# Kernel tuning notes

Hardware: AMD Instinct MI355X
Metric: run time of the kernel (lower is better)

## Reference

```python
import jax, jax.numpy as jnp
import numpy as np

N_NODES = 50000
N_EDGES = 640000
D = 128


def setup_inputs() -> dict:
    key = jax.random.key(0)
    ks = jax.random.split(key, 8)
    nfeats = jax.random.normal(ks[0], (N_NODES, 1, D), dtype=jnp.float32)
    efeats = jax.random.normal(ks[1], (N_EDGES, 1, D), dtype=jnp.float32)
    # Linear params (PyTorch convention: weight [out, in])
    W_msg_w = jax.random.normal(ks[2], (D, 2 * D), dtype=jnp.float32) * 0.05
    W_msg_b = jax.random.normal(ks[3], (D,), dtype=jnp.float32) * 0.05
    W_apply_w = jax.random.normal(ks[4], (D, 2 * D), dtype=jnp.float32) * 0.05
    W_apply_b = jax.random.normal(ks[5], (D,), dtype=jnp.float32) * 0.05
    src = jax.random.randint(ks[6], (N_EDGES,), 0, N_NODES, dtype=jnp.int32)
    dst = jax.random.randint(ks[7], (N_EDGES,), 0, N_NODES, dtype=jnp.int32)
    return {
        "nfeats": nfeats, "efeats": efeats,
        "W_msg_w": W_msg_w, "W_msg_b": W_msg_b,
        "W_apply_w": W_apply_w, "W_apply_b": W_apply_b,
        "src": src, "dst": dst,
    }


def reference(nfeats, efeats, W_msg_w, W_msg_b, W_apply_w, W_apply_b, src, dst):
    n_nodes = nfeats.shape[0]
    # message: W_msg(cat[src_h, edge_h])  -> [E, 1, D_out]
    msg_in = jnp.concatenate([nfeats[src], efeats], axis=-1)  # [E,1,2D]
    m = jnp.einsum("eqi,oi->eqo", msg_in, W_msg_w) + W_msg_b
    # segment-mean over destination nodes (DGL fn.mean; zero for isolated nodes)
    sums = jax.ops.segment_sum(m, dst, num_segments=n_nodes)  # [N,1,D]
    counts = jax.ops.segment_sum(jnp.ones((m.shape[0],), m.dtype), dst,
                                 num_segments=n_nodes)  # [N]
    h_neigh = sums / jnp.maximum(counts, 1.0)[:, None, None]
    # apply: relu(W_apply(cat[h, h_neigh]))
    upd_in = jnp.concatenate([nfeats, h_neigh], axis=-1)  # [N,1,2D]
    out = jax.nn.relu(jnp.einsum("nqi,oi->nqo", upd_in, W_apply_w) + W_apply_b)
    return out
```

## Files before the change

kernel.cpp:

```cpp
#include <hip/hip_runtime.h>

#define D 128
#define TWO_D 256
#define LDSR 264

typedef __attribute__((ext_vector_type(4))) float f32x4;
typedef __attribute__((ext_vector_type(8))) short bf16x8;

static __device__ __forceinline__ unsigned short f2bf(float x) {
  union { float f; unsigned u; } v; v.f = x;
  unsigned r = (v.u + 0x7fffu + ((v.u >> 16) & 1u)) >> 16;
  return (unsigned short)r;
}

__global__ void prep_pack(const float* __restrict__ wmsg,
                          const float* __restrict__ wapp,
                          unsigned short* __restrict__ Wp,
                          int* __restrict__ counts, int n_nodes) {
  int p = blockIdx.x * blockDim.x + threadIdx.x;
  int j = p & 7;
  int lane = (p >> 3) & 63;
  int ot = (p >> 9) & 7;
  int k0i = (p >> 12) & 7;
  int g = p >> 15;
  int o = ot * 16 + (lane & 15);
  int k = k0i * 32 + (lane >> 4) * 8 + j;
  const float* W = g ? wapp : wmsg;
  Wp[p] = f2bf(W[o * 256 + k]);
  if (p < n_nodes) counts[p] = 0;
}

__global__ void hist_kernel(const int* __restrict__ dst, int* __restrict__ counts,
                            int n_edges) {
  int e = blockIdx.x * blockDim.x + threadIdx.x;
  if (e < n_edges) atomicAdd(&counts[dst[e]], 1);
}

__global__ void scan_kernel(const int* __restrict__ counts, int* __restrict__ offsets,
                            int* __restrict__ cursor, int n, int n_edges) {
  __shared__ int lds[1024];
  int t = threadIdx.x;
  int C = (n + 1023) / 1024;
  int beg = t * C;
  int end = beg + C; if (end > n) end = n;
  int s = 0;
  for (int i = beg; i < end; ++i) s += counts[i];
  lds[t] = s;
  __syncthreads();
  for (int off = 1; off < 1024; off <<= 1) {
    int v = (t >= off) ? lds[t - off] : 0;
    __syncthreads();
    lds[t] += v;
    __syncthreads();
  }
  int run = (t == 0) ? 0 : lds[t - 1];
  for (int i = beg; i < end; ++i) {
    offsets[i] = run;
    cursor[i] = run;
    run += counts[i];
  }
  if (t == 1023) offsets[n] = n_edges;
}

__global__ void scatter_kernel(const int* __restrict__ dst, int* __restrict__ cursor,
                               int* __restrict__ edge_list, int n_edges) {
  int e = blockIdx.x * blockDim.x + threadIdx.x;
  if (e < n_edges) {
    int p = atomicAdd(&cursor[dst[e]], 1);
    edge_list[p] = e;
  }
}

__global__ __launch_bounds__(256) void gather_kernel(
    const float* __restrict__ nfeats, const float* __restrict__ efeats,
    const int* __restrict__ src, const int* __restrict__ edge_list,
    const int* __restrict__ offsets, unsigned short* __restrict__ X1,
    int n_nodes) {
  int w = (blockIdx.x * 256 + threadIdx.x) >> 6;
  int lane = threadIdx.x & 63;
  if (w >= n_nodes) return;
  int beg = offsets[w], end = offsets[w + 1];
  int cnt = end - beg;
  const f32x4* nf4 = (const f32x4*)nfeats;
  const f32x4* ef4 = (const f32x4*)efeats;
  const int c32 = lane & 31;
  const int slot = lane >> 5;
  f32x4 accn = (f32x4){0.f, 0.f, 0.f, 0.f};
  f32x4 acce = (f32x4){0.f, 0.f, 0.f, 0.f};

  for (int j0 = beg; j0 < end; j0 += 64) {
    int nj = end - j0; if (nj > 64) nj = 64;
    int e = 0, s = 0;
    if (lane < nj) { e = edge_list[j0 + lane]; s = src[e]; }
    for (int p = 0; p < nj; p += 4) {
      int i0 = p + slot;
      int i1 = p + 2 + slot;
      int ee0 = __shfl(e, i0), ss0 = __shfl(s, i0);
      int ee1 = __shfl(e, i1), ss1 = __shfl(s, i1);
      bool v0 = i0 < nj, v1 = i1 < nj;
      f32x4 a0, b0, a1, b1;
      if (v0) {
        a0 = nf4[(size_t)ss0 * 32 + c32];
        b0 = __builtin_nontemporal_load(&ef4[(size_t)ee0 * 32 + c32]);
      }
      if (v1) {
        a1 = nf4[(size_t)ss1 * 32 + c32];
        b1 = __builtin_nontemporal_load(&ef4[(size_t)ee1 * 32 + c32]);
      }
      if (v0) { accn += a0; acce += b0; }
      if (v1) { accn += a1; acce += b1; }
    }
  }
  #pragma unroll
  for (int k = 0; k < 4; ++k) {
    accn[k] += __shfl_xor(accn[k], 32);
    acce[k] += __shfl_xor(acce[k], 32);
  }
  float inv = (cnt > 0) ? 1.0f / (float)cnt : 0.0f;
  f32x4 v = (lane < 32) ? accn : acce;
  ushort4 o;
  o.x = f2bf(v[0] * inv); o.y = f2bf(v[1] * inv);
  o.z = f2bf(v[2] * inv); o.w = f2bf(v[3] * inv);
  ((ushort4*)(X1 + (size_t)w * TWO_D))[lane] = o;
}

__global__ __launch_bounds__(256) void node_gemm(
    const unsigned short* __restrict__ X1,
    const unsigned short* __restrict__ Wp,
    const float* __restrict__ b1,
    const float* __restrict__ b2,
    const float* __restrict__ nfeats,
    const int* __restrict__ offsets,
    float* __restrict__ out,
    int n_nodes) {
  __shared__ unsigned short xt[64 * LDSR];
  __shared__ int cnts[64];
  const int tid = threadIdx.x;
  const int base = blockIdx.x * 64;

  if (tid < 64) {
    int g = base + tid;
    cnts[tid] = (g < n_nodes) ? (offsets[g + 1] - offsets[g]) : 0;
  }
  #pragma unroll
  for (int it = 0; it < 8; ++it) {
    int chunk = tid + it * 256;
    int r = chunk >> 5, c = chunk & 31;
    int g = base + r;
    uint4 v = make_uint4(0, 0, 0, 0);
    if (g < n_nodes) v = ((const uint4*)X1)[(size_t)g * 32 + c];
    *(uint4*)&xt[r * LDSR + c * 8] = v;
  }
  __syncthreads();

  const int lane = tid & 63;
  const int wid = tid >> 6;
  const int m16 = lane & 15;
  const int quad = lane >> 4;
  const int arow = wid * 16 + m16;
  const int lane8 = lane << 3;

  f32x4 acc[8];
  #pragma unroll
  for (int ot = 0; ot < 8; ++ot) acc[ot] = (f32x4){0.f, 0.f, 0.f, 0.f};

  #pragma unroll
  for (int k0i = 0; k0i < 8; ++k0i) {
    bf16x8 a = *(const bf16x8*)&xt[arow * LDSR + k0i * 32 + quad * 8];
    #pragma unroll
    for (int ot = 0; ot < 8; ++ot) {
      bf16x8 b = *(const bf16x8*)&Wp[((k0i * 8 + ot) << 9) + lane8];
      acc[ot] = __builtin_amdgcn_mfma_f32_16x16x32_bf16(a, b, acc[ot], 0, 0, 0);
    }
  }
  __syncthreads();

  #pragma unroll
  for (int ot = 0; ot < 8; ++ot) {
    int o = ot * 16 + m16;
    float bias = b1[o];
    #pragma unroll
    for (int r = 0; r < 4; ++r) {
      int m = wid * 16 + quad * 4 + r;
      float h = acc[ot][r] + (cnts[m] > 0 ? bias : 0.0f);
      xt[m * LDSR + 128 + o] = f2bf(h);
    }
  }
  #pragma unroll
  for (int it = 0; it < 8; ++it) {
    int chunk = tid + it * 256;
    int r = chunk >> 5, c = chunk & 31;
    int g = base + r;
    float4 v = make_float4(0.f, 0.f, 0.f, 0.f);
    if (g < n_nodes) v = ((const float4*)nfeats)[(size_t)g * 32 + c];
    ushort4 bv;
    bv.x = f2bf(v.x); bv.y = f2bf(v.y); bv.z = f2bf(v.z); bv.w = f2bf(v.w);
    *(ushort4*)&xt[r * LDSR + c * 4] = bv;
  }
  __syncthreads();

  #pragma unroll
  for (int ot = 0; ot < 8; ++ot) acc[ot] = (f32x4){0.f, 0.f, 0.f, 0.f};

  #pragma unroll
  for (int k0i = 0; k0i < 8; ++k0i) {
    bf16x8 a = *(const bf16x8*)&xt[arow * LDSR + k0i * 32 + quad * 8];
    #pragma unroll
    for (int ot = 0; ot < 8; ++ot) {
      bf16x8 b = *(const bf16x8*)&Wp[32768 + ((k0i * 8 + ot) << 9) + lane8];
      acc[ot] = __builtin_amdgcn_mfma_f32_16x16x32_bf16(a, b, acc[ot], 0, 0, 0);
    }
  }
  #pragma unroll
  for (int ot = 0; ot < 8; ++ot) {
    int o = ot * 16 + m16;
    float bias = b2[o];
    #pragma unroll
    for (int r = 0; r < 4; ++r) {
      int m = wid * 16 + quad * 4 + r;
      int g = base + m;
      if (g < n_nodes) {
        float v = acc[ot][r] + bias;
        out[(size_t)g * D + o] = v > 0.f ? v : 0.f;
      }
    }
  }
}

extern "C" void kernel_launch(void* const* d_in, const int* in_sizes, int n_in,
                              void* d_out, int out_size, void* d_ws, size_t ws_size,
                              hipStream_t stream) {
  const float* nfeats = (const float*)d_in[0];
  const float* efeats = (const float*)d_in[1];
  const float* Wmsg_f = (const float*)d_in[2];
  const float* b1     = (const float*)d_in[3];
  const float* Wapp_f = (const float*)d_in[4];
  const float* b2     = (const float*)d_in[5];
  const int*   src    = (const int*)d_in[6];
  const int*   dst    = (const int*)d_in[7];
  const int n_nodes = in_sizes[0] / D;
  const int n_edges = in_sizes[6];

  char* ws = (char*)d_ws;
  size_t off = 0;
  unsigned short* X1 = (unsigned short*)(ws + off); off += (size_t)n_nodes * TWO_D * 2;
  unsigned short* Wp = (unsigned short*)(ws + off); off += (size_t)2 * D * TWO_D * 2;
  int* counts    = (int*)(ws + off); off += (size_t)n_nodes * 4;
  int* offsets   = (int*)(ws + off); off += (size_t)(n_nodes + 1) * 4;
  int* cursor    = (int*)(ws + off); off += (size_t)n_nodes * 4;
  int* edge_list = (int*)(ws + off); off += (size_t)n_edges * 4;
  (void)ws_size; (void)n_in; (void)out_size;

  prep_pack<<<256, 256, 0, stream>>>(Wmsg_f, Wapp_f, Wp, counts, n_nodes);
  hist_kernel<<<(n_edges + 255) / 256, 256, 0, stream>>>(dst, counts, n_edges);
  scan_kernel<<<1, 1024, 0, stream>>>(counts, offsets, cursor, n_nodes, n_edges);
  scatter_kernel<<<(n_edges + 255) / 256, 256, 0, stream>>>(dst, cursor, edge_list, n_edges);
  gather_kernel<<<(n_nodes + 3) / 4, 256, 0, stream>>>(nfeats, efeats, src, edge_list, offsets, X1, n_nodes);
  node_gemm<<<(n_nodes + 63) / 64, 256, 0, stream>>>(X1, Wp, b1, b2, nfeats, offsets, (float*)d_out, n_nodes);
}
```

Baseline: 689.4 us.

## Fuse gather into node GEMM and reuse histogram atomics for CSR scatter

Merges the per-node gather/mean kernel into the node GEMM kernel, so the mean features are written straight to shared memory and the intermediate bf16 X1 buffer round trip through global memory goes away. The histogram pass now records each edge's atomic rank, so the scatter needs no second atomic pass and no cursor array. Edge ids are stored together with their src index as int2 pairs, which removes the dependent src lookup in the gather loop. The trade-off is lower parallelism in the gather phase: each wave now handles 16 nodes in sequence inside a block that also holds a large LDS tile, which may reduce latency hiding.

```diff
diff --git a/kernel.cpp b/kernel.cpp
--- a/kernel.cpp
+++ b/kernel.cpp
@@ -30,14 +30,14 @@
   if (p < n_nodes) counts[p] = 0;
 }
 
-__global__ void hist_kernel(const int* __restrict__ dst, int* __restrict__ counts,
-                            int n_edges) {
+__global__ void hist_rank_kernel(const int* __restrict__ dst, int* __restrict__ counts,
+                                 int* __restrict__ rank, int n_edges) {
   int e = blockIdx.x * blockDim.x + threadIdx.x;
-  if (e < n_edges) atomicAdd(&counts[dst[e]], 1);
+  if (e < n_edges) rank[e] = atomicAdd(&counts[dst[e]], 1);
 }
 
 __global__ void scan_kernel(const int* __restrict__ counts, int* __restrict__ offsets,
-                            int* __restrict__ cursor, int n, int n_edges) {
+                            int n, int n_edges) {
   __shared__ int lds[1024];
   int t = threadIdx.x;
   int C = (n + 1023) / 1024;
@@ -56,105 +56,86 @@
   int run = (t == 0) ? 0 : lds[t - 1];
   for (int i = beg; i < end; ++i) {
     offsets[i] = run;
-    cursor[i] = run;
     run += counts[i];
   }
   if (t == 1023) offsets[n] = n_edges;
 }
 
-__global__ void scatter_kernel(const int* __restrict__ dst, int* __restrict__ cursor,
-                               int* __restrict__ edge_list, int n_edges) {
+__global__ void scatter_kernel(const int* __restrict__ dst, const int* __restrict__ src,
+                               const int* __restrict__ rank,
+                               const int* __restrict__ offsets,
+                               int2* __restrict__ edge_list, int n_edges) {
   int e = blockIdx.x * blockDim.x + threadIdx.x;
   if (e < n_edges) {
-    int p = atomicAdd(&cursor[dst[e]], 1);
-    edge_list[p] = e;
-  }
-}
-
-__global__ __launch_bounds__(256) void gather_kernel(
+    int d = dst[e];
+    edge_list[offsets[d] + rank[e]] = make_int2(e, src[e]);
+  }
+}
+
+__global__ __launch_bounds__(256) void gcn_fused(
     const float* __restrict__ nfeats, const float* __restrict__ efeats,
-    const int* __restrict__ src, const int* __restrict__ edge_list,
-    const int* __restrict__ offsets, unsigned short* __restrict__ X1,
-    int n_nodes) {
-  int w = (blockIdx.x * 256 + threadIdx.x) >> 6;
-  int lane = threadIdx.x & 63;
-  if (w >= n_nodes) return;
-  int beg = offsets[w], end = offsets[w + 1];
-  int cnt = end - beg;
+    const int2* __restrict__ edge_list, const int* __restrict__ offsets,
+    const unsigned short* __restrict__ Wp,
+    const float* __restrict__ b1, const float* __restrict__ b2,
+    float* __restrict__ out, int n_nodes) {
+  __shared__ unsigned short xt[64 * LDSR];
+  __shared__ int cnts[64];
+  const int tid = threadIdx.x;
+  const int base = blockIdx.x * 64;
+  const int lane = tid & 63;
+  const int wid = tid >> 6;
+
   const f32x4* nf4 = (const f32x4*)nfeats;
   const f32x4* ef4 = (const f32x4*)efeats;
   const int c32 = lane & 31;
   const int slot = lane >> 5;
-  f32x4 accn = (f32x4){0.f, 0.f, 0.f, 0.f};
-  f32x4 acce = (f32x4){0.f, 0.f, 0.f, 0.f};
-
-  for (int j0 = beg; j0 < end; j0 += 64) {
-    int nj = end - j0; if (nj > 64) nj = 64;
-    int e = 0, s = 0;
-    if (lane < nj) { e = edge_list[j0 + lane]; s = src[e]; }
-    for (int p = 0; p < nj; p += 4) {
-      int i0 = p + slot;
-      int i1 = p + 2 + slot;
-      int ee0 = __shfl(e, i0), ss0 = __shfl(s, i0);
-      int ee1 = __shfl(e, i1), ss1 = __shfl(s, i1);
-      bool v0 = i0 < nj, v1 = i1 < nj;
-      f32x4 a0, b0, a1, b1;
-      if (v0) {
-        a0 = nf4[(size_t)ss0 * 32 + c32];
-        b0 = __builtin_nontemporal_load(&ef4[(size_t)ee0 * 32 + c32]);
+
+  for (int i = 0; i < 16; ++i) {
+    int m = wid * 16 + i;
+    int g = base + m;
+    if (g >= n_nodes) break;
+    int beg = offsets[g], end = offsets[g + 1];
+    int cnt = end - beg;
+    f32x4 accn = (f32x4){0.f, 0.f, 0.f, 0.f};
+    f32x4 acce = (f32x4){0.f, 0.f, 0.f, 0.f};
+    for (int j0 = beg; j0 < end; j0 += 64) {
+      int nj = end - j0; if (nj > 64) nj = 64;
+      int e = 0, s = 0;
+      if (lane < nj) { int2 es = edge_list[j0 + lane]; e = es.x; s = es.y; }
+      for (int p = 0; p < nj; p += 4) {
+        int i0 = p + slot;
+        int i1 = p + 2 + slot;
+        int ee0 = __shfl(e, i0), ss0 = __shfl(s, i0);
+        int ee1 = __shfl(e, i1), ss1 = __shfl(s, i1);
+        bool v0 = i0 < nj, v1 = i1 < nj;
+        f32x4 a0, b0, a1, b1v;
+        if (v0) {
+          a0 = nf4[(size_t)ss0 * 32 + c32];
+          b0 = __builtin_nontemporal_load(&ef4[(size_t)ee0 * 32 + c32]);
+        }
+        if (v1) {
+          a1 = nf4[(size_t)ss1 * 32 + c32];
+          b1v = __builtin_nontemporal_load(&ef4[(size_t)ee1 * 32 + c32]);
+        }
+        if (v0) { accn += a0; acce += b0; }
+        if (v1) { accn += a1; acce += b1v; }
       }
-      if (v1) {
-        a1 = nf4[(size_t)ss1 * 32 + c32];
-        b1 = __builtin_nontemporal_load(&ef4[(size_t)ee1 * 32 + c32]);
-      }
-      if (v0) { accn += a0; acce += b0; }
-      if (v1) { accn += a1; acce += b1; }
-    }
-  }
-  #pragma unroll
-  for (int k = 0; k < 4; ++k) {
-    accn[k] += __shfl_xor(accn[k], 32);
-    acce[k] += __shfl_xor(acce[k], 32);
-  }
-  float inv = (cnt > 0) ? 1.0f / (float)cnt : 0.0f;
-  f32x4 v = (lane < 32) ? accn : acce;
-  ushort4 o;
-  o.x = f2bf(v[0] * inv); o.y = f2bf(v[1] * inv);
-  o.z = f2bf(v[2] * inv); o.w = f2bf(v[3] * inv);
-  ((ushort4*)(X1 + (size_t)w * TWO_D))[lane] = o;
-}
-
-__global__ __launch_bounds__(256) void node_gemm(
-    const unsigned short* __restrict__ X1,
-    const unsigned short* __restrict__ Wp,
-    const float* __restrict__ b1,
-    const float* __restrict__ b2,
-    const float* __restrict__ nfeats,
-    const int* __restrict__ offsets,
-    float* __restrict__ out,
-    int n_nodes) {
-  __shared__ unsigned short xt[64 * LDSR];
-  __shared__ int cnts[64];
-  const int tid = threadIdx.x;
-  const int base = blockIdx.x * 64;
-
-  if (tid < 64) {
-    int g = base + tid;
-    cnts[tid] = (g < n_nodes) ? (offsets[g + 1] - offsets[g]) : 0;
-  }
-  #pragma unroll
-  for (int it = 0; it < 8; ++it) {
-    int chunk = tid + it * 256;
-    int r = chunk >> 5, c = chunk & 31;
-    int g = base + r;
-    uint4 v = make_uint4(0, 0, 0, 0);
-    if (g < n_nodes) v = ((const uint4*)X1)[(size_t)g * 32 + c];
-    *(uint4*)&xt[r * LDSR + c * 8] = v;
-  }
-  __syncthreads();
-
-  const int lane = tid & 63;
-  const int wid = tid >> 6;
+    }
+    #pragma unroll
+    for (int k = 0; k < 4; ++k) {
+      accn[k] += __shfl_xor(accn[k], 32);
+      acce[k] += __shfl_xor(acce[k], 32);
+    }
+    float inv = (cnt > 0) ? 1.0f / (float)cnt : 0.0f;
+    f32x4 v = (lane < 32) ? accn : acce;
+    ushort4 o;
+    o.x = f2bf(v[0] * inv); o.y = f2bf(v[1] * inv);
+    o.z = f2bf(v[2] * inv); o.w = f2bf(v[3] * inv);
+    *(ushort4*)&xt[m * LDSR + lane * 4] = o;
+    if (lane == 0) cnts[m] = cnt;
+  }
+  __syncthreads();
+
   const int m16 = lane & 15;
   const int quad = lane >> 4;
   const int arow = wid * 16 + m16;
@@ -243,18 +224,16 @@
 
   char* ws = (char*)d_ws;
   size_t off = 0;
-  unsigned short* X1 = (unsigned short*)(ws + off); off += (size_t)n_nodes * TWO_D * 2;
   unsigned short* Wp = (unsigned short*)(ws + off); off += (size_t)2 * D * TWO_D * 2;
   int* counts    = (int*)(ws + off); off += (size_t)n_nodes * 4;
   int* offsets   = (int*)(ws + off); off += (size_t)(n_nodes + 1) * 4;
-  int* cursor    = (int*)(ws + off); off += (size_t)n_nodes * 4;
-  int* edge_list = (int*)(ws + off); off += (size_t)n_edges * 4;
+  int* rank      = (int*)(ws + off); off += (size_t)n_edges * 4;
+  int2* edge_list = (int2*)(ws + off); off += (size_t)n_edges * 8;
   (void)ws_size; (void)n_in; (void)out_size;
 
   prep_pack<<<256, 256, 0, stream>>>(Wmsg_f, Wapp_f, Wp, counts, n_nodes);
-  hist_kernel<<<(n_edges + 255) / 256, 256, 0, stream>>>(dst, counts, n_edges);
-  scan_kernel<<<1, 1024, 0, stream>>>(counts, offsets, cursor, n_nodes, n_edges);
-  scatter_kernel<<<(n_edges + 255) / 256, 256, 0, stream>>>(dst, cursor, edge_list, n_edges);
-  gather_kernel<<<(n_nodes + 3) / 4, 256, 0, stream>>>(nfeats, efeats, src, edge_list, offsets, X1, n_nodes);
-  node_gemm<<<(n_nodes + 63) / 64, 256, 0, stream>>>(X1, Wp, b1, b2, nfeats, offsets, (float*)d_out, n_nodes);
-}
+  hist_rank_kernel<<<(n_edges + 255) / 256, 256, 0, stream>>>(dst, counts, rank, n_edges);
+  scan_kernel<<<1, 1024, 0, stream>>>(counts, offsets, n_nodes, n_edges);
+  scatter_kernel<<<(n_edges + 255) / 256, 256, 0, stream>>>(dst, src, rank, offsets, edge_list, n_edges);
+  gcn_fused<<<(n_nodes + 63) / 64, 256, 0, stream>>>(nfeats, efeats, edge_list, offsets, Wp, b1, b2, (float*)d_out, n_nodes);
+}
```

Result: faster. 617.9 us (-10.4%).

## Parallelize CSR scan, record atomic ranks, pack src into edge list, prefetch gather loads

Applied to the files above, without the earlier changes.

The histogram pass now stores each edge's atomic rank, so the scatter can place edges without a second atomic cursor pass. The single-block serial scan becomes a two-pass multi-block scan. The edge list stores (edge, src) pairs, which removes a dependent src lookup in the gather. The gather loop also software-prefetches the next group of feature rows to overlap load latency. In exchange there is an extra rank buffer, a wider edge list and one more small kernel launch.

```diff
diff --git a/kernel.cpp b/kernel.cpp
--- a/kernel.cpp
+++ b/kernel.cpp
@@ -30,52 +30,74 @@
   if (p < n_nodes) counts[p] = 0;
 }
 
-__global__ void hist_kernel(const int* __restrict__ dst, int* __restrict__ counts,
-                            int n_edges) {
+__global__ void hist_rank_kernel(const int* __restrict__ dst, int* __restrict__ counts,
+                                 int* __restrict__ rank, int n_edges) {
   int e = blockIdx.x * blockDim.x + threadIdx.x;
-  if (e < n_edges) atomicAdd(&counts[dst[e]], 1);
-}
-
-__global__ void scan_kernel(const int* __restrict__ counts, int* __restrict__ offsets,
-                            int* __restrict__ cursor, int n, int n_edges) {
-  __shared__ int lds[1024];
-  int t = threadIdx.x;
-  int C = (n + 1023) / 1024;
-  int beg = t * C;
-  int end = beg + C; if (end > n) end = n;
+  if (e < n_edges) rank[e] = atomicAdd(&counts[dst[e]], 1);
+}
+
+__global__ void scan_part(const int* __restrict__ counts, int* __restrict__ partial,
+                          int n) {
+  __shared__ int lds[256];
+  int b = blockIdx.x, t = threadIdx.x;
+  int g0 = b * 1024 + t * 4;
   int s = 0;
-  for (int i = beg; i < end; ++i) s += counts[i];
+  #pragma unroll
+  for (int j = 0; j < 4; ++j) { int g = g0 + j; if (g < n) s += counts[g]; }
   lds[t] = s;
   __syncthreads();
-  for (int off = 1; off < 1024; off <<= 1) {
+  for (int off = 128; off > 0; off >>= 1) {
+    if (t < off) lds[t] += lds[t + off];
+    __syncthreads();
+  }
+  if (t == 0) partial[b] = lds[0];
+}
+
+__global__ void scan_write(const int* __restrict__ counts, const int* __restrict__ partial,
+                           int* __restrict__ offsets, int n, int n_edges, int nb) {
+  __shared__ int lds[256];
+  __shared__ int pb[64];
+  int b = blockIdx.x, t = threadIdx.x;
+  if (t < nb) pb[t] = partial[t];
+  __syncthreads();
+  int base = 0;
+  for (int k = 0; k < b; ++k) base += pb[k];
+  int g0 = b * 1024 + t * 4;
+  int c0 = (g0 + 0 < n) ? counts[g0 + 0] : 0;
+  int c1 = (g0 + 1 < n) ? counts[g0 + 1] : 0;
+  int c2 = (g0 + 2 < n) ? counts[g0 + 2] : 0;
+  int c3 = (g0 + 3 < n) ? counts[g0 + 3] : 0;
+  lds[t] = c0 + c1 + c2 + c3;
+  __syncthreads();
+  for (int off = 1; off < 256; off <<= 1) {
     int v = (t >= off) ? lds[t - off] : 0;
     __syncthreads();
     lds[t] += v;
     __syncthreads();
   }
-  int run = (t == 0) ? 0 : lds[t - 1];
-  for (int i = beg; i < end; ++i) {
-    offsets[i] = run;
-    cursor[i] = run;
-    run += counts[i];
-  }
-  if (t == 1023) offsets[n] = n_edges;
-}
-
-__global__ void scatter_kernel(const int* __restrict__ dst, int* __restrict__ cursor,
-                               int* __restrict__ edge_list, int n_edges) {
+  int texc = base + ((t > 0) ? lds[t - 1] : 0);
+  if (g0 + 0 < n) offsets[g0 + 0] = texc;
+  if (g0 + 1 < n) offsets[g0 + 1] = texc + c0;
+  if (g0 + 2 < n) offsets[g0 + 2] = texc + c0 + c1;
+  if (g0 + 3 < n) offsets[g0 + 3] = texc + c0 + c1 + c2;
+  if (b == 0 && t == 0) offsets[n] = n_edges;
+}
+
+__global__ void scatter_kernel(const int* __restrict__ dst, const int* __restrict__ src,
+                               const int* __restrict__ rank,
+                               const int* __restrict__ offsets,
+                               int2* __restrict__ edge_list, int n_edges) {
   int e = blockIdx.x * blockDim.x + threadIdx.x;
   if (e < n_edges) {
-    int p = atomicAdd(&cursor[dst[e]], 1);
-    edge_list[p] = e;
+    int d = dst[e];
+    edge_list[offsets[d] + rank[e]] = make_int2(e, src[e]);
   }
 }
 
 __global__ __launch_bounds__(256) void gather_kernel(
     const float* __restrict__ nfeats, const float* __restrict__ efeats,
-    const int* __restrict__ src, const int* __restrict__ edge_list,
-    const int* __restrict__ offsets, unsigned short* __restrict__ X1,
-    int n_nodes) {
+    const int2* __restrict__ edge_list, const int* __restrict__ offsets,
+    unsigned short* __restrict__ X1, int n_nodes) {
   int w = (blockIdx.x * 256 + threadIdx.x) >> 6;
   int lane = threadIdx.x & 63;
   if (w >= n_nodes) return;
@@ -91,24 +113,29 @@
   for (int j0 = beg; j0 < end; j0 += 64) {
     int nj = end - j0; if (nj > 64) nj = 64;
     int e = 0, s = 0;
-    if (lane < nj) { e = edge_list[j0 + lane]; s = src[e]; }
+    if (lane < nj) { int2 es = edge_list[j0 + lane]; e = es.x; s = es.y; }
+    int i0 = slot, i1 = 2 + slot;
+    int ee0 = __shfl(e, i0), ss0 = __shfl(s, i0);
+    int ee1 = __shfl(e, i1), ss1 = __shfl(s, i1);
+    bool v0 = i0 < nj, v1 = i1 < nj;
+    f32x4 a0 = (f32x4){0.f,0.f,0.f,0.f}, b0 = a0, a1 = a0, b1v = a0;
+    if (v0) { a0 = nf4[(size_t)ss0 * 32 + c32];
+              b0 = __builtin_nontemporal_load(&ef4[(size_t)ee0 * 32 + c32]); }
+    if (v1) { a1 = nf4[(size_t)ss1 * 32 + c32];
+              b1v = __builtin_nontemporal_load(&ef4[(size_t)ee1 * 32 + c32]); }
     for (int p = 0; p < nj; p += 4) {
-      int i0 = p + slot;
-      int i1 = p + 2 + slot;
-      int ee0 = __shfl(e, i0), ss0 = __shfl(s, i0);
-      int ee1 = __shfl(e, i1), ss1 = __shfl(s, i1);
-      bool v0 = i0 < nj, v1 = i1 < nj;
-      f32x4 a0, b0, a1, b1;
-      if (v0) {
-        a0 = nf4[(size_t)ss0 * 32 + c32];
-        b0 = __builtin_nontemporal_load(&ef4[(size_t)ee0 * 32 + c32]);
-      }
-      if (v1) {
-        a1 = nf4[(size_t)ss1 * 32 + c32];
-        b1 = __builtin_nontemporal_load(&ef4[(size_t)ee1 * 32 + c32]);
-      }
+      int n0 = (p + 4 + slot) & 63, n1 = (p + 6 + slot) & 63;
+      int eeN0 = __shfl(e, n0), ssN0 = __shfl(s, n0);
+      int eeN1 = __shfl(e, n1), ssN1 = __shfl(s, n1);
+      bool w0 = p + 4 + slot < nj, w1 = p + 6 + slot < nj;
+      f32x4 aN0 = (f32x4){0.f,0.f,0.f,0.f}, bN0 = aN0, aN1 = aN0, bN1 = aN0;
+      if (w0) { aN0 = nf4[(size_t)ssN0 * 32 + c32];
+                bN0 = __builtin_nontemporal_load(&ef4[(size_t)eeN0 * 32 + c32]); }
+      if (w1) { aN1 = nf4[(size_t)ssN1 * 32 + c32];
+                bN1 = __builtin_nontemporal_load(&ef4[(size_t)eeN1 * 32 + c32]); }
       if (v0) { accn += a0; acce += b0; }
-      if (v1) { accn += a1; acce += b1; }
+      if (v1) { accn += a1; acce += b1v; }
+      a0 = aN0; b0 = bN0; a1 = aN1; b1v = bN1; v0 = w0; v1 = w1;
     }
   }
   #pragma unroll
@@ -240,6 +267,7 @@
   const int*   dst    = (const int*)d_in[7];
   const int n_nodes = in_sizes[0] / D;
   const int n_edges = in_sizes[6];
+  const int nb = (n_nodes + 1023) / 1024;
 
   char* ws = (char*)d_ws;
   size_t off = 0;
@@ -247,14 +275,16 @@
   unsigned short* Wp = (unsigned short*)(ws + off); off += (size_t)2 * D * TWO_D * 2;
   int* counts    = (int*)(ws + off); off += (size_t)n_nodes * 4;
   int* offsets   = (int*)(ws + off); off += (size_t)(n_nodes + 1) * 4;
-  int* cursor    = (int*)(ws + off); off += (size_t)n_nodes * 4;
-  int* edge_list = (int*)(ws + off); off += (size_t)n_edges * 4;
+  int* rank      = (int*)(ws + off); off += (size_t)n_edges * 4;
+  int* partial   = (int*)(ws + off); off += 64 * 4;
+  int2* edge_list = (int2*)(ws + off); off += (size_t)n_edges * 8;
   (void)ws_size; (void)n_in; (void)out_size;
 
   prep_pack<<<256, 256, 0, stream>>>(Wmsg_f, Wapp_f, Wp, counts, n_nodes);
-  hist_kernel<<<(n_edges + 255) / 256, 256, 0, stream>>>(dst, counts, n_edges);
-  scan_kernel<<<1, 1024, 0, stream>>>(counts, offsets, cursor, n_nodes, n_edges);
-  scatter_kernel<<<(n_edges + 255) / 256, 256, 0, stream>>>(dst, cursor, edge_list, n_edges);
-  gather_kernel<<<(n_nodes + 3) / 4, 256, 0, stream>>>(nfeats, efeats, src, edge_list, offsets, X1, n_nodes);
+  hist_rank_kernel<<<(n_edges + 255) / 256, 256, 0, stream>>>(dst, counts, rank, n_edges);
+  scan_part<<<nb, 256, 0, stream>>>(counts, partial, n_nodes);
+  scan_write<<<nb, 256, 0, stream>>>(counts, partial, offsets, n_nodes, n_edges, nb);
+  scatter_kernel<<<(n_edges + 255) / 256, 256, 0, stream>>>(dst, src, rank, offsets, edge_list, n_edges);
+  gather_kernel<<<(n_nodes + 3) / 4, 256, 0, stream>>>(nfeats, efeats, edge_list, offsets, X1, n_nodes);
   node_gemm<<<(n_nodes + 63) / 64, 256, 0, stream>>>(X1, Wp, b1, b2, nfeats, offsets, (float*)d_out, n_nodes);
 }
```

Result: faster. 556.0 us (-19.3%).
